# Kernel tuning notes

Measured on AMD Instinct MI355X. Metric: run time of the kernel, lower is better.

## Reference

```python
import jax, jax.numpy as jnp
import numpy as np

B, S, H, NH, DH, F, L = 4, 2048, 512, 8, 64, 2048, 4
ALPHA = 1.0   # config.lag_time_scale_alpha
EPS = 1e-12   # BERT layer_norm_eps
MS_PER_MIN = 60.0 * 1000.0


def setup_inputs() -> dict:
    key = jax.random.key(0)
    ks = jax.random.split(key, 24)
    p = lambda k, shape: (jax.random.normal(k, shape, jnp.float32) * 0.02)
    inp = {
        "query_states": jax.random.normal(ks[0], (B, S, H), jnp.float32),
        "attention_mask": jnp.zeros((B, 1, 1, S), jnp.float32),
        "position_bias": jax.random.normal(ks[1], (1, NH, S, S), jnp.float32) * 0.02,
        "timestamp": jnp.sort(jax.random.randint(ks[2], (B, S), 0, 36_000_000, jnp.int32), axis=-1),
        # stacked per-layer parameters (L leading dim)
        "wq": p(ks[3], (L, H, H)), "bq": jnp.zeros((L, H), jnp.float32),
        "wk": p(ks[4], (L, H, H)), "bk": jnp.zeros((L, H), jnp.float32),
        "wv": p(ks[5], (L, H, H)), "bv": jnp.zeros((L, H), jnp.float32),
        "wo": p(ks[6], (L, H, H)), "bo": jnp.zeros((L, H), jnp.float32),
        "ln1_g": jnp.ones((L, H), jnp.float32), "ln1_b": jnp.zeros((L, H), jnp.float32),
        "wi": p(ks[7], (L, H, F)), "bi": jnp.zeros((L, F), jnp.float32),
        "wo2": p(ks[8], (L, F, H)), "bo2": jnp.zeros((L, H), jnp.float32),
        "ln2_g": jnp.ones((L, H), jnp.float32), "ln2_b": jnp.zeros((L, H), jnp.float32),
    }
    return inp


def _ln(x, g, b):
    m = x.mean(-1, keepdims=True)
    v = ((x - m) ** 2).mean(-1, keepdims=True)
    return (x - m) / jnp.sqrt(v + EPS) * g + b


def reference(query_states, attention_mask, position_bias, timestamp,
              wq, bq, wk, bk, wv, bv, wo, bo, ln1_g, ln1_b,
              wi, bi, wo2, bo2, ln2_g, ln2_b):
    # encoder (is_decoder=False) lag-time scale: (B,1,S,S)
    lag = (timestamp[:, None, :, None] - timestamp[:, None, None, :]).astype(jnp.float32) / MS_PER_MIN
    scale = np.sqrt(DH).astype(np.float32) - ALPHA / (jnp.clip(lag, 0.0) + 1.0) + ALPHA

    x = query_states
    for l in range(L):
        def proj(w, b):
            return (x @ w + b).reshape(B, S, NH, DH).transpose(0, 2, 1, 3)  # (B,NH,S,DH)
        q, k, v = proj(wq[l], bq[l]), proj(wk[l], bk[l]), proj(wv[l], bv[l])
        scores = jnp.einsum('bhqd,bhkd->bhqk', q, k) / scale + position_bias + attention_mask
        probs = jax.nn.softmax(scores, axis=-1)
        ctx = jnp.einsum('bhqk,bhkd->bhqd', probs, v).transpose(0, 2, 1, 3).reshape(B, S, H)
        attn = _ln(ctx @ wo[l] + bo[l] + x, ln1_g[l], ln1_b[l])
        ffn = jax.nn.gelu(attn @ wi[l] + bi[l], approximate=False) @ wo2[l] + bo2[l]
        x = _ln(ffn + attn, ln2_g[l], ln2_b[l])
    return x
```

## Files before the change

kernel.cpp:

```cpp
#include <hip/hip_runtime.h>
#include <stdint.h>

typedef unsigned short u16;
using half8   = __attribute__((ext_vector_type(8))) _Float16;
using half4v  = __attribute__((ext_vector_type(4))) _Float16;
using half2v  = __attribute__((ext_vector_type(2))) _Float16;
using float4v = __attribute__((ext_vector_type(4))) float;

#define L2E 1.4426950408889634f

__device__ inline float4v f4zero() { float4v z = {0.f, 0.f, 0.f, 0.f}; return z; }

__device__ inline u16 f2h(float f) {
  union { _Float16 h; u16 u; } v; v.h = (_Float16)f; return v.u;
}
__device__ inline float h2f(u16 u) {
  union { u16 u; _Float16 h; } v; v.u = u; return (float)v.h;
}

__device__ inline half2v cvtpk(float a, float b) {
  return __builtin_bit_cast(half2v, __builtin_amdgcn_cvt_pkrtz(a, b));
}
__device__ inline _Float16 hexp2_(_Float16 x) {
  _Float16 r;
  asm("v_exp_f16 %0, %1" : "=v"(r) : "v"(x));
  return r;
}
__device__ inline float fdot2f(half2v a, float c) {
#if __has_builtin(__builtin_amdgcn_fdot2)
  typedef __attribute__((ext_vector_type(2))) __fp16 h2r;
  return __builtin_amdgcn_fdot2(__builtin_bit_cast(h2r, a),
                                __builtin_bit_cast(h2r, 0x3C003C00u), c, false);
#else
  return c + (float)a.x + (float)a.y;
#endif
}

__device__ inline void glds16(const u16* g, u16* lds_base, int lane) {
#if __has_builtin(__builtin_amdgcn_global_load_lds)
  (void)lane;
  __builtin_amdgcn_global_load_lds((const __attribute__((address_space(1))) void*)g,
                                   (__attribute__((address_space(3))) void*)lds_base,
                                   16, 0, 0);
#else
  *(uint4*)(lds_base + (size_t)lane * 8) = *(const uint4*)g;
#endif
}

__global__ __launch_bounds__(256) void transpose_cast_kernel(
    const float* __restrict__ in, u16* __restrict__ out, int K, int N, size_t out_ls) {
  __shared__ float tile[32][33];
  const int tx = threadIdx.x & 31, ty = threadIdx.x >> 5;
  in  += (size_t)blockIdx.z * K * N;
  out += (size_t)blockIdx.z * out_ls;
  const int n  = blockIdx.x * 32 + tx;
  const int k0 = blockIdx.y * 32;
#pragma unroll
  for (int j = 0; j < 32; j += 8)
    tile[ty + j][tx] = in[(size_t)(k0 + ty + j) * N + n];
  __syncthreads();
  const int k = k0 + tx;
  const int n0 = blockIdx.x * 32;
#pragma unroll
  for (int j = 0; j < 32; j += 8)
    out[(size_t)(n0 + ty + j) * K + k] = f2h(tile[tx][ty + j]);
}

__global__ __launch_bounds__(256) void cast_kernel(const float* __restrict__ in,
                                                   u16* __restrict__ out) {
  const int i = (blockIdx.x * 256 + threadIdx.x) * 4;
  float4 t = *(const float4*)(in + i);
  ushort4 o;
  o.x = f2h(t.x); o.y = f2h(t.y); o.z = f2h(t.z); o.w = f2h(t.w);
  *(ushort4*)(out + i) = o;
}

__global__ __launch_bounds__(256) void pb_tile_kernel(const float* __restrict__ pb,
                                                      u16* __restrict__ pbT) {
  const int g  = blockIdx.x * 256 + threadIdx.x;
  const int mm = g & 15;
  const int q  = (g >> 4) & 2047;
  const int kbh = g >> 15;
  const int kb = kbh & 31, h = kbh >> 5;
  const float* src = pb + ((size_t)h * 2048 + q) * 2048 + kb * 64 + mm;
  ushort4 o;
  o.x = f2h(src[0]  * L2E);
  o.y = f2h(src[16] * L2E);
  o.z = f2h(src[32] * L2E);
  o.w = f2h(src[48] * L2E);
  *(ushort4*)(pbT + ((size_t)(h * 32 + kb) * 2048 + q) * 64 + mm * 4) = o;
}

__global__ __launch_bounds__(256) void inv_tile_kernel(const int* __restrict__ ts,
                                                       u16* __restrict__ invT) {
  const int g  = blockIdx.x * 256 + threadIdx.x;
  const int mm = g & 15;
  const int q  = (g >> 4) & 2047;
  const int kb = (g >> 15) & 31;
  const int b  = g >> 20;
  const int tq = ts[b * 2048 + q];
  ushort4 o;
  u16* op = (u16*)&o;
#pragma unroll
  for (int nb = 0; nb < 4; nb++) {
    const int k = kb * 64 + nb * 16 + mm;
    const int du = tq - ts[b * 2048 + k];
    const float u = (du > 0) ? (float)du : 0.f;
    op[nb] = f2h(fmaf(u, L2E, 86561.70245333781f) *
                 __builtin_amdgcn_rcpf(fmaf(u, 9.f, 480000.f)));
  }
  *(ushort4*)(invT + ((size_t)(b * 32 + kb) * 2048 + q) * 64 + mm * 4) = o;
}

__global__ __launch_bounds__(256) void maskts_kernel(const float* __restrict__ mask,
                                                     const int* __restrict__ ts,
                                                     float* __restrict__ maskE,
                                                     float* __restrict__ tsf) {
  const int i = blockIdx.x * 256 + threadIdx.x;
  maskE[i] = mask[i] * L2E;
  tsf[i]   = (float)ts[i];
}

template <int BM, int BN, int NN, int KK, int EPI>
__global__ __launch_bounds__(256) void gemm_kernel(
    const u16* __restrict__ A, const u16* __restrict__ Wt,
    const float* __restrict__ b0, const float* __restrict__ b1, const float* __restrict__ b2,
    const u16* __restrict__ resid,
    void* __restrict__ o0, void* __restrict__ o1, void* __restrict__ o2) {
  constexpr int FI = BM / 32;
  constexpr int FJB = BN / 32;
  constexpr int FIW = BM / 32;
  constexpr int FJW = BN / 32;
  constexpr int NT = KK / 64;
  __shared__ __align__(16) u16 smem[2 * BM * 64 + 2 * BN * 64];
  u16* As0 = smem;
  u16* Bs0 = smem + 2 * BM * 64;
  const int tid = threadIdx.x, lane = tid & 63, wv = tid >> 6;
  const int quad = lane >> 4, mm = lane & 15;
  const int m0 = blockIdx.x * BM, n0 = blockIdx.y * BN;
  const int wm = (wv >> 1) * (BM / 2), wn = (wv & 1) * (BN / 2);
  const int srow = tid >> 3, slot = tid & 7;
  const int chunk = slot ^ (srow & 7);
  const u16* Ag = A  + (size_t)(m0 + srow) * KK + chunk * 8;
  const u16* Bg = Wt + (size_t)(n0 + srow) * KK + chunk * 8;
  const int sw = mm & 7;

  float4v acc[FIW][FJW];
#pragma unroll
  for (int i = 0; i < FIW; i++)
#pragma unroll
    for (int j = 0; j < FJW; j++) acc[i][j] = f4zero();

#pragma unroll
  for (int i = 0; i < FI; i++)
    glds16(Ag + (size_t)i * 32 * KK, As0 + (size_t)(wv * 8 + i * 32) * 64, lane);
#pragma unroll
  for (int j = 0; j < FJB; j++)
    glds16(Bg + (size_t)j * 32 * KK, Bs0 + (size_t)(wv * 8 + j * 32) * 64, lane);

  int cur = 0;
#pragma unroll 2
  for (int kt = 0; kt < NT; kt++) {
    __syncthreads();

    if (kt + 1 < NT) {
      const size_t ko = (size_t)(kt + 1) * 64;
#pragma unroll
      for (int i = 0; i < FI; i++)
        glds16(Ag + (size_t)i * 32 * KK + ko,
               As0 + (size_t)(cur ^ 1) * BM * 64 + (size_t)(wv * 8 + i * 32) * 64, lane);
#pragma unroll
      for (int j = 0; j < FJB; j++)
        glds16(Bg + (size_t)j * 32 * KK + ko,
               Bs0 + (size_t)(cur ^ 1) * BN * 64 + (size_t)(wv * 8 + j * 32) * 64, lane);
    }

    const u16* Ac = As0 + (size_t)cur * BM * 64;
    const u16* Bc = Bs0 + (size_t)cur * BN * 64;
#pragma unroll
    for (int ks = 0; ks < 2; ks++) {
      half8 a[FIW], b[FJW];
#pragma unroll
      for (int i = 0; i < FIW; i++)
        a[i] = *(const half8*)(Ac + (size_t)(wm + i * 16 + mm) * 64 + (size_t)((ks * 4 + quad) ^ sw) * 8);
#pragma unroll
      for (int j = 0; j < FJW; j++)
        b[j] = *(const half8*)(Bc + (size_t)(wn + j * 16 + mm) * 64 + (size_t)((ks * 4 + quad) ^ sw) * 8);
#pragma unroll
      for (int i = 0; i < FIW; i++)
#pragma unroll
        for (int j = 0; j < FJW; j++)
          acc[i][j] = __builtin_amdgcn_mfma_f32_16x16x32_f16(a[i], b[j], acc[i][j], 0, 0, 0);
    }
    cur ^= 1;
  }

  if constexpr (EPI == 4) {
    if (n0 >= 1024) {
      __syncthreads();
      u16* T = smem;
      const int h0 = (n0 >> 6) & 7;
      const int b_ = m0 >> 11, s_base = m0 & 2047;
#pragma unroll
      for (int j = 0; j < FJW; j++) {
        const int cn = wn + j * 16 + mm;
        const float bias = b2[(n0 & 511) + cn];
#pragma unroll
        for (int i = 0; i < FIW; i++)
#pragma unroll
          for (int r = 0; r < 4; r++) {
            const int gl = wm + i * 16 + quad * 4 + r;
            T[gl * 130 + cn] = f2h(acc[i][j][r] + bias);
          }
      }
      __syncthreads();
      const int rr = tid >> 1, shalf = tid & 1;
      const int hh = rr >> 6, dd = rr & 63;
      u16* outp = (u16*)o2 + ((size_t)((b_ * 8 + h0 + hh) * 64 + dd)) * 2048
                + s_base + shalf * 64;
#pragma unroll
      for (int g = 0; g < 8; g++) {
        union { u16 u[8]; uint4 v; } pk;
#pragma unroll
        for (int e = 0; e < 8; e++) {
          const int inner = g * 8 + e;
          const int sl = shalf * 64 + (((inner & 3) << 4) | (inner >> 2));
          pk.u[e] = T[sl * 130 + rr];
        }
        *(uint4*)(outp + g * 8) = pk.v;
      }
      return;
    }
  }

#pragma unroll
  for (int j = 0; j < FJW; j++) {
    const int gn = n0 + wn + j * 16 + mm;
    if (EPI == 4) {
      const int which = gn >> 9, col = gn & 511, h = (gn >> 6) & 7, d = gn & 63;
      const float* bp = (which == 0) ? b0 : b1;
      const float bias = bp[col];
      u16* dst = (which == 0) ? (u16*)o0 : (u16*)o1;
#pragma unroll
      for (int i = 0; i < FIW; i++)
#pragma unroll
        for (int r = 0; r < 4; r++) {
          const int gm = m0 + wm + i * 16 + quad * 4 + r;
          const int b_ = gm >> 11, s_ = gm & 2047;
          const float val = acc[i][j][r] + bias;
          dst[((size_t)((b_ * 8 + h) * 2048 + s_)) * 64 + d] = f2h(val);
        }
    } else {
      const float bias = b0[gn];
#pragma unroll
      for (int i = 0; i < FIW; i++)
#pragma unroll
        for (int r = 0; r < 4; r++) {
          const int gm = m0 + wm + i * 16 + quad * 4 + r;
          const float val = acc[i][j][r] + bias;
          const size_t idx = (size_t)gm * NN + gn;
          if (EPI == 2) {
            ((float*)o0)[idx] = val + h2f(resid[idx]);
          } else {
            const float z  = val * 0.70710678118654752f;
            const float az = fabsf(z);
            const float t  = __builtin_amdgcn_rcpf(1.0f + 0.3275911f * az);
            const float poly = t * (0.254829592f + t * (-0.284496736f +
                               t * (1.421413741f + t * (-1.453152027f + t * 1.061405429f))));
            const float e = __builtin_amdgcn_exp2f(-az * az * L2E);
            float erf_ = 1.0f - poly * e;
            erf_ = (z < 0.0f) ? -erf_ : erf_;
            ((u16*)o0)[idx] = f2h(val * 0.5f * (1.0f + erf_));
          }
        }
    }
  }
}

template <int TILED>
__global__ __launch_bounds__(512) void flash4_kernel(
    const u16* __restrict__ Q, const u16* __restrict__ Kb, const u16* __restrict__ Vt,
    const u16* __restrict__ pbT, const u16* __restrict__ invT,
    const float* __restrict__ pb32,
    const float* __restrict__ maskE, const float* __restrict__ tsf,
    u16* __restrict__ ctx) {
  __shared__ __align__(16) u16 Kls[2][64 * 64];
  __shared__ __align__(16) u16 Vls[2][64 * 64];
  __shared__ __align__(16) u16 P[8][16 * 64];
  const int tid = threadIdx.x, lane = tid & 63, w = tid >> 6;
  const int quad = lane >> 4, mm = lane & 15;
  const int bh = blockIdx.y, b_ = bh >> 3, h_ = bh & 7;
  const int q0 = blockIdx.x * 128 + w * 16;
  const size_t qk_base = (size_t)bh * 2048 * 64;
  const size_t v_base  = (size_t)bh * 64 * 2048;
  const int srow = lane >> 3, slot = lane & 7;
  const int chunk = slot ^ srow;
  const int sw = mm & 7;

  const u16* Kgl = Kb + qk_base + (size_t)(w * 8 + srow) * 64 + chunk * 8;
  const u16* Vgl = Vt + v_base + (size_t)(w * 8 + srow) * 2048 + chunk * 8;

  glds16(Kgl, &Kls[0][(w * 8) * 64], lane);
  glds16(Vgl, &Vls[0][(w * 8) * 64], lane);

  half8 aq[2];
#pragma unroll
  for (int t = 0; t < 2; t++)
    aq[t] = *(const half8*)(Q + qk_base + (size_t)(q0 + mm) * 64 + t * 32 + quad * 8);

  float tqf[4];
  if (TILED < 2) {
#pragma unroll
    for (int r = 0; r < 4; r++) tqf[r] = tsf[b_ * 2048 + q0 + quad * 4 + r];
  }

  float l_r[4] = {0.f, 0.f, 0.f, 0.f};
  float4v o[4];
#pragma unroll
  for (int ob = 0; ob < 4; ob++) o[ob] = f4zero();

  ushort4 pbc[4], invc[4]; float tkc[4], mkc[4];
  if (TILED >= 1) {
#pragma unroll
    for (int r = 0; r < 4; r++)
      pbc[r] = *(const ushort4*)(pbT + ((size_t)(h_ * 32) * 2048 + q0 + quad * 4 + r) * 64 + mm * 4);
  }
  if (TILED == 2) {
#pragma unroll
    for (int r = 0; r < 4; r++)
      invc[r] = *(const ushort4*)(invT + ((size_t)(b_ * 32) * 2048 + q0 + quad * 4 + r) * 64 + mm * 4);
  } else {
#pragma unroll
    for (int nb = 0; nb < 4; nb++) tkc[nb] = tsf[b_ * 2048 + nb * 16 + mm];
  }
#pragma unroll
  for (int nb = 0; nb < 4; nb++) mkc[nb] = maskE[b_ * 2048 + nb * 16 + mm];

  int cur = 0;
  for (int kt = 0; kt < 32; kt++) {
    const int k0 = kt * 64;
    __syncthreads();

    const int kn = (kt < 31) ? kt + 1 : kt;
    ushort4 pbn[4], invn[4]; float tkn[4], mkn[4];
    if (TILED >= 1) {
#pragma unroll
      for (int r = 0; r < 4; r++)
        pbn[r] = *(const ushort4*)(pbT + ((size_t)(h_ * 32 + kn) * 2048 + q0 + quad * 4 + r) * 64 + mm * 4);
    }
    if (TILED == 2) {
#pragma unroll
      for (int r = 0; r < 4; r++)
        invn[r] = *(const ushort4*)(invT + ((size_t)(b_ * 32 + kn) * 2048 + q0 + quad * 4 + r) * 64 + mm * 4);
    } else {
#pragma unroll
      for (int nb = 0; nb < 4; nb++) tkn[nb] = tsf[b_ * 2048 + kn * 64 + nb * 16 + mm];
    }
#pragma unroll
    for (int nb = 0; nb < 4; nb++) mkn[nb] = maskE[b_ * 2048 + kn * 64 + nb * 16 + mm];

    if (kt < 31) {
      const size_t ko = (size_t)(kt + 1) * 4096;
      const size_t vo = (size_t)(kt + 1) * 64;
      glds16(Kgl + ko, &Kls[cur ^ 1][(w * 8) * 64], lane);
      glds16(Vgl + vo, &Vls[cur ^ 1][(w * 8) * 64], lane);
    }

    const u16* Kc = Kls[cur];
    float4v s[4];
    __builtin_amdgcn_s_setprio(1);
#pragma unroll
    for (int nb = 0; nb < 4; nb++) {
      const half8 kf0 = *(const half8*)(Kc + (size_t)(nb * 16 + mm) * 64 + (size_t)(quad ^ sw) * 8);
      const half8 kf1 = *(const half8*)(Kc + (size_t)(nb * 16 + mm) * 64 + (size_t)((4 + quad) ^ sw) * 8);
      s[nb] = __builtin_amdgcn_mfma_f32_16x16x32_f16(aq[0], kf0, f4zero(), 0, 0, 0);
      s[nb] = __builtin_amdgcn_mfma_f32_16x16x32_f16(aq[1], kf1, s[nb], 0, 0, 0);
    }
    __builtin_amdgcn_s_setprio(0);

    const half2v mk01 = cvtpk(mkc[0], mkc[1]);
    const half2v mk23 = cvtpk(mkc[2], mkc[3]);
#pragma unroll
    for (int r = 0; r < 4; r++) {
      half2v pb01, pb23, iv01, iv23;
      if (TILED >= 1) {
        pb01 = *(const half2v*)&pbc[r].x;
        pb23 = *(const half2v*)&pbc[r].z;
      } else {
        float pv[4];
#pragma unroll
        for (int nb = 0; nb < 4; nb++)
          pv[nb] = pb32[((size_t)h_ * 2048 + q0 + quad * 4 + r) * 2048 + k0 + nb * 16 + mm] * L2E;
        pb01 = cvtpk(pv[0], pv[1]); pb23 = cvtpk(pv[2], pv[3]);
      }
      if (TILED == 2) {
        iv01 = *(const half2v*)&invc[r].x;
        iv23 = *(const half2v*)&invc[r].z;
      } else {
        float ivv[4];
#pragma unroll
        for (int nb = 0; nb < 4; nb++) {
          const float u = fmaxf(tqf[r] - tkc[nb], 0.f);
          ivv[nb] = fmaf(u, L2E, 86561.70245333781f) *
                    __builtin_amdgcn_rcpf(fmaf(u, 9.f, 480000.f));
        }
        iv01 = cvtpk(ivv[0], ivv[1]); iv23 = cvtpk(ivv[2], ivv[3]);
      }
      const half2v s01 = cvtpk(s[0][r], s[1][r]);
      const half2v s23 = cvtpk(s[2][r], s[3][r]);
      const half2v t01 = __builtin_elementwise_fma(s01, iv01, pb01 + mk01);
      const half2v t23 = __builtin_elementwise_fma(s23, iv23, pb23 + mk23);
      half2v p01, p23;
      p01.x = hexp2_(t01.x); p01.y = hexp2_(t01.y);
      p23.x = hexp2_(t23.x); p23.y = hexp2_(t23.y);
      l_r[r] = fdot2f(p01, l_r[r]);
      l_r[r] = fdot2f(p23, l_r[r]);
      const int prow = quad * 4 + r;
      union { half2v h2[2]; half4v h4; } uu;
      uu.h2[0] = p01; uu.h2[1] = p23;
      *(half4v*)((char*)P[w] + prow * 128 + ((mm * 8) ^ ((prow & 7) << 4))) = uu.h4;
    }

    const u16* Vc = Vls[cur];
    const char* Pb = (const char*)P[w] + mm * 128;
    const int pxor = (mm & 7) << 4;
    const half8 ap0 = *(const half8*)(Pb + ((quad * 16) ^ pxor));
    const half8 ap1 = *(const half8*)(Pb + ((64 + quad * 16) ^ pxor));
    __builtin_amdgcn_s_setprio(1);
#pragma unroll
    for (int ob = 0; ob < 4; ob++) {
      const half8 vf0 = *(const half8*)(Vc + (size_t)(ob * 16 + mm) * 64 + (size_t)(quad ^ sw) * 8);
      const half8 vf1 = *(const half8*)(Vc + (size_t)(ob * 16 + mm) * 64 + (size_t)((4 + quad) ^ sw) * 8);
      o[ob] = __builtin_amdgcn_mfma_f32_16x16x32_f16(ap0, vf0, o[ob], 0, 0, 0);
      o[ob] = __builtin_amdgcn_mfma_f32_16x16x32_f16(ap1, vf1, o[ob], 0, 0, 0);
    }
    __builtin_amdgcn_s_setprio(0);

#pragma unroll
    for (int r = 0; r < 4; r++) { pbc[r] = pbn[r]; invc[r] = invn[r]; }
#pragma unroll
    for (int nb = 0; nb < 4; nb++) { tkc[nb] = tkn[nb]; mkc[nb] = mkn[nb]; }
    cur ^= 1;
  }

#pragma unroll
  for (int r = 0; r < 4; r++) {
    float l = l_r[r];
#pragma unroll
    for (int sh = 1; sh < 16; sh <<= 1) l += __shfl_xor(l, sh, 64);
    const float rl = __builtin_amdgcn_rcpf(l);
    const int qrow = q0 + quad * 4 + r;
#pragma unroll
    for (int ob = 0; ob < 4; ob++)
      ctx[((size_t)b_ * 2048 + qrow) * 512 + h_ * 64 + ob * 16 + mm] = f2h(o[ob][r] * rl);
  }
}

__global__ __launch_bounds__(256) void ln_kernel(
    const float* __restrict__ in, const float* __restrict__ g, const float* __restrict__ bb,
    float* __restrict__ of, u16* __restrict__ obf) {
  const int lane = threadIdx.x & 63, w = threadIdx.x >> 6;
  const int row = blockIdx.x * 4 + w;
  const float* x = in + (size_t)row * 512;
  float v[8];
  const float4 t0 = *(const float4*)(x + lane * 8);
  const float4 t1 = *(const float4*)(x + lane * 8 + 4);
  v[0] = t0.x; v[1] = t0.y; v[2] = t0.z; v[3] = t0.w;
  v[4] = t1.x; v[5] = t1.y; v[6] = t1.z; v[7] = t1.w;
  float s = 0.f;
#pragma unroll
  for (int i = 0; i < 8; i++) s += v[i];
#pragma unroll
  for (int sh = 1; sh < 64; sh <<= 1) s += __shfl_xor(s, sh, 64);
  const float mean = s * (1.0f / 512.0f);
  float sq = 0.f;
#pragma unroll
  for (int i = 0; i < 8; i++) { const float d = v[i] - mean; sq += d * d; }
#pragma unroll
  for (int sh = 1; sh < 64; sh <<= 1) sq += __shfl_xor(sq, sh, 64);
  const float rstd = rsqrtf(sq * (1.0f / 512.0f) + 1e-12f);
#pragma unroll
  for (int i = 0; i < 8; i++) {
    const int col = lane * 8 + i;
    const float y = (v[i] - mean) * rstd * g[col] + bb[col];
    if (of) of[(size_t)row * 512 + col] = y;
    obf[(size_t)row * 512 + col] = f2h(y);
  }
}

extern "C" void kernel_launch(void* const* d_in, const int* in_sizes, int n_in,
                              void* d_out, int out_size, void* d_ws, size_t ws_size,
                              hipStream_t stream) {
  const float* x_in = (const float*)d_in[0];
  const float* mask = (const float*)d_in[1];
  const float* pb   = (const float*)d_in[2];
  const int*   ts   = (const int*)d_in[3];
  const float* wq = (const float*)d_in[4];  const float* bq = (const float*)d_in[5];
  const float* wk = (const float*)d_in[6];  const float* bk = (const float*)d_in[7];
  const float* wvp = (const float*)d_in[8]; const float* bv = (const float*)d_in[9];
  const float* wo = (const float*)d_in[10]; const float* bo = (const float*)d_in[11];
  const float* ln1g = (const float*)d_in[12]; const float* ln1b = (const float*)d_in[13];
  const float* wi = (const float*)d_in[14]; const float* bi = (const float*)d_in[15];
  const float* wo2 = (const float*)d_in[16]; const float* bo2 = (const float*)d_in[17];
  const float* ln2g = (const float*)d_in[18]; const float* ln2b = (const float*)d_in[19];

  char* ws = (char*)d_ws;
  const size_t o_wqkv  = 0;
  const size_t o_woT   = 6291456;
  const size_t o_wiT   = 8388608;
  const size_t o_wo2T  = 16777216;
  const size_t o_maskE = 25165824;
  const size_t o_tsf   = 25198592;
  const size_t o_xbf   = 25231360;
  const size_t o_qb    = 33619968;
  const size_t o_kb    = 42008576;
  const size_t o_vb    = 50397184;
  const size_t o_ctx   = 58785792;
  const size_t o_attnb = 67174400;
  const size_t o_tmp   = 75563008;
  const size_t o_pbT   = 92340224;
  const size_t o_invT  = 159449088;
  const int tiled = (ws_size >= o_invT + 33554432ull) ? 2
                  : (ws_size >= o_pbT + 67108864ull) ? 1 : 0;

  u16*   wqkvT = (u16*)(ws + o_wqkv);
  u16*   woT   = (u16*)(ws + o_woT);
  u16*   wiT   = (u16*)(ws + o_wiT);
  u16*   wo2T  = (u16*)(ws + o_wo2T);
  float* maskE = (float*)(ws + o_maskE);
  float* tsf   = (float*)(ws + o_tsf);
  u16*   xbf   = (u16*)(ws + o_xbf);
  u16*   qb    = (u16*)(ws + o_qb);
  u16*   kb    = (u16*)(ws + o_kb);
  u16*   vb    = (u16*)(ws + o_vb);
  u16*   ctx   = (u16*)(ws + o_ctx);
  u16*   hb    = (u16*)(ws + o_qb);
  u16*   attnb = (u16*)(ws + o_attnb);
  float* tmp   = (float*)(ws + o_tmp);
  u16*   pbT   = (u16*)(ws + o_pbT);
  u16*   invT  = (u16*)(ws + o_invT);

  const dim3 blk(256);
  const dim3 blk512(512);
  transpose_cast_kernel<<<dim3(16, 16, 4), blk, 0, stream>>>(wq,  wqkvT,          512, 512, 786432);
  transpose_cast_kernel<<<dim3(16, 16, 4), blk, 0, stream>>>(wk,  wqkvT + 262144, 512, 512, 786432);
  transpose_cast_kernel<<<dim3(16, 16, 4), blk, 0, stream>>>(wvp, wqkvT + 524288, 512, 512, 786432);
  transpose_cast_kernel<<<dim3(16, 16, 4), blk, 0, stream>>>(wo,  woT,  512, 512,  262144);
  transpose_cast_kernel<<<dim3(64, 16, 4), blk, 0, stream>>>(wi,  wiT,  512, 2048, 1048576);
  transpose_cast_kernel<<<dim3(16, 64, 4), blk, 0, stream>>>(wo2, wo2T, 2048, 512, 1048576);
  maskts_kernel<<<32, blk, 0, stream>>>(mask, ts, maskE, tsf);
  cast_kernel<<<4096, blk, 0, stream>>>(x_in, xbf);
  if (tiled >= 1) pb_tile_kernel<<<32768, blk, 0, stream>>>(pb, pbT);
  if (tiled == 2) inv_tile_kernel<<<16384, blk, 0, stream>>>(ts, invT);

  for (int l = 0; l < 4; l++) {
    gemm_kernel<128, 128, 1536, 512, 4><<<dim3(64, 12), blk, 0, stream>>>(
        xbf, wqkvT + (size_t)l * 786432, bq + l * 512, bk + l * 512, bv + l * 512,
        nullptr, qb, kb, vb);
    if (tiled == 2)
      flash4_kernel<2><<<dim3(16, 32), blk512, 0, stream>>>(qb, kb, vb, pbT, invT, pb, maskE, tsf, ctx);
    else if (tiled == 1)
      flash4_kernel<1><<<dim3(16, 32), blk512, 0, stream>>>(qb, kb, vb, pbT, nullptr, pb, maskE, tsf, ctx);
    else
      flash4_kernel<0><<<dim3(16, 32), blk512, 0, stream>>>(qb, kb, vb, nullptr, nullptr, pb, maskE, tsf, ctx);
    gemm_kernel<128, 64, 512, 512, 2><<<dim3(64, 8), blk, 0, stream>>>(
        ctx, woT + (size_t)l * 262144, bo + l * 512, nullptr, nullptr, xbf,
        tmp, nullptr, nullptr);
    ln_kernel<<<2048, blk, 0, stream>>>(tmp, ln1g + l * 512, ln1b + l * 512, nullptr, attnb);
    gemm_kernel<128, 128, 2048, 512, 3><<<dim3(64, 16), blk, 0, stream>>>(
        attnb, wiT + (size_t)l * 1048576, bi + l * 2048, nullptr, nullptr, nullptr,
        hb, nullptr, nullptr);
    gemm_kernel<128, 64, 512, 2048, 2><<<dim3(64, 8), blk, 0, stream>>>(
        hb, wo2T + (size_t)l * 1048576, bo2 + l * 512, nullptr, nullptr, attnb,
        tmp, nullptr, nullptr);
    ln_kernel<<<2048, blk, 0, stream>>>(tmp, ln2g + l * 512, ln2b + l * 512,
                                        (l == 3) ? (float*)d_out : nullptr, xbf);
  }
  (void)in_sizes; (void)n_in; (void)out_size;
}
```

Measured before the change: 1.159 ms.

## Add 256x128-tile 512-thread GEMM for QKV and FFN-up projections

Adds a new gemm8_kernel that uses 8 waves and a 256x128 output tile (each wave computing 64x64) for the QKV projection and the FFN up-projection. The old kernel's V-transpose epilogue is split into two half passes through shared memory. The goal is more operand reuse per LDS load and fewer blocks. The trade-offs are higher register pressure, half as many blocks (384/512), and a single-buffered K loop with two barriers per step instead of the previous double buffering, which may expose load latency.

Result: faster. 1.123 ms (-3.1%).

```diff
diff --git a/kernel.cpp b/kernel.cpp
--- a/kernel.cpp
+++ b/kernel.cpp
@@ -195,85 +195,166 @@
     cur ^= 1;
   }
 
+#pragma unroll
+  for (int j = 0; j < FJW; j++) {
+    const int gn = n0 + wn + j * 16 + mm;
+    const float bias = b0[gn];
+#pragma unroll
+    for (int i = 0; i < FIW; i++)
+#pragma unroll
+      for (int r = 0; r < 4; r++) {
+        const int gm = m0 + wm + i * 16 + quad * 4 + r;
+        const float val = acc[i][j][r] + bias;
+        const size_t idx = (size_t)gm * NN + gn;
+        if (EPI == 2) {
+          ((float*)o0)[idx] = val + h2f(resid[idx]);
+        } else {
+          const float z  = val * 0.70710678118654752f;
+          const float az = fabsf(z);
+          const float t  = __builtin_amdgcn_rcpf(1.0f + 0.3275911f * az);
+          const float poly = t * (0.254829592f + t * (-0.284496736f +
+                             t * (1.421413741f + t * (-1.453152027f + t * 1.061405429f))));
+          const float e = __builtin_amdgcn_exp2f(-az * az * L2E);
+          float erf_ = 1.0f - poly * e;
+          erf_ = (z < 0.0f) ? -erf_ : erf_;
+          ((u16*)o0)[idx] = f2h(val * 0.5f * (1.0f + erf_));
+        }
+      }
+  }
+  (void)b1; (void)b2; (void)o1; (void)o2;
+}
+
+template <int NN, int KK, int EPI>
+__global__ __launch_bounds__(512) void gemm8_kernel(
+    const u16* __restrict__ A, const u16* __restrict__ Wt,
+    const float* __restrict__ b0, const float* __restrict__ b1, const float* __restrict__ b2,
+    void* __restrict__ o0, void* __restrict__ o1, void* __restrict__ o2) {
+  __shared__ __align__(16) u16 smem[256 * 64 + 128 * 64];
+  u16* As = smem;
+  u16* Bs = smem + 256 * 64;
+  const int tid = threadIdx.x, lane = tid & 63, wv = tid >> 6;
+  const int quad = lane >> 4, mm = lane & 15;
+  const int m0 = blockIdx.x * 256, n0 = blockIdx.y * 128;
+  const int wm = (wv >> 1) * 64, wn = (wv & 1) * 64;
+  const int srow = tid >> 3, slot = tid & 7;
+  const int chunk = slot ^ (srow & 7);
+  const u16* Ag = A  + (size_t)(m0 + srow) * KK + chunk * 8;
+  const u16* Bg = Wt + (size_t)(n0 + srow) * KK + chunk * 8;
+  const int sw = mm & 7;
+
+  float4v acc[4][4];
+#pragma unroll
+  for (int i = 0; i < 4; i++)
+#pragma unroll
+    for (int j = 0; j < 4; j++) acc[i][j] = f4zero();
+
+  for (int kte = 0; kte < KK; kte += 64) {
+#pragma unroll
+    for (int p = 0; p < 4; p++)
+      glds16(Ag + (size_t)(p * 64) * KK + kte, As + (size_t)(p * 64 + wv * 8) * 64, lane);
+#pragma unroll
+    for (int p = 0; p < 2; p++)
+      glds16(Bg + (size_t)(p * 64) * KK + kte, Bs + (size_t)(p * 64 + wv * 8) * 64, lane);
+    __syncthreads();
+
+#pragma unroll
+    for (int ks = 0; ks < 2; ks++) {
+      half8 a[4], b[4];
+#pragma unroll
+      for (int i = 0; i < 4; i++)
+        a[i] = *(const half8*)(As + (size_t)(wm + i * 16 + mm) * 64 + (size_t)((ks * 4 + quad) ^ sw) * 8);
+#pragma unroll
+      for (int j = 0; j < 4; j++)
+        b[j] = *(const half8*)(Bs + (size_t)(wn + j * 16 + mm) * 64 + (size_t)((ks * 4 + quad) ^ sw) * 8);
+#pragma unroll
+      for (int i = 0; i < 4; i++)
+#pragma unroll
+        for (int j = 0; j < 4; j++)
+          acc[i][j] = __builtin_amdgcn_mfma_f32_16x16x32_f16(a[i], b[j], acc[i][j], 0, 0, 0);
+    }
+    __syncthreads();
+  }
+
   if constexpr (EPI == 4) {
     if (n0 >= 1024) {
-      __syncthreads();
+      const int b_ = m0 >> 11, s_base = m0 & 2047;
+      const int h0 = (n0 >> 6) & 7;
       u16* T = smem;
-      const int h0 = (n0 >> 6) & 7;
-      const int b_ = m0 >> 11, s_base = m0 & 2047;
-#pragma unroll
-      for (int j = 0; j < FJW; j++) {
-        const int cn = wn + j * 16 + mm;
-        const float bias = b2[(n0 & 511) + cn];
-#pragma unroll
-        for (int i = 0; i < FIW; i++)
-#pragma unroll
-          for (int r = 0; r < 4; r++) {
-            const int gl = wm + i * 16 + quad * 4 + r;
-            T[gl * 130 + cn] = f2h(acc[i][j][r] + bias);
+#pragma unroll
+      for (int hp = 0; hp < 2; hp++) {
+        __syncthreads();
+        if ((wv >> 2) == hp) {
+          const int lm = wm & 127;
+#pragma unroll
+          for (int j = 0; j < 4; j++) {
+            const int cn = wn + j * 16 + mm;
+            const float bias = b2[(n0 & 511) + cn];
+#pragma unroll
+            for (int i = 0; i < 4; i++)
+#pragma unroll
+              for (int r = 0; r < 4; r++)
+                T[(lm + i * 16 + quad * 4 + r) * 130 + cn] = f2h(acc[i][j][r] + bias);
           }
-      }
-      __syncthreads();
-      const int rr = tid >> 1, shalf = tid & 1;
-      const int hh = rr >> 6, dd = rr & 63;
-      u16* outp = (u16*)o2 + ((size_t)((b_ * 8 + h0 + hh) * 64 + dd)) * 2048
-                + s_base + shalf * 64;
-#pragma unroll
-      for (int g = 0; g < 8; g++) {
-        union { u16 u[8]; uint4 v; } pk;
-#pragma unroll
-        for (int e = 0; e < 8; e++) {
-          const int inner = g * 8 + e;
-          const int sl = shalf * 64 + (((inner & 3) << 4) | (inner >> 2));
-          pk.u[e] = T[sl * 130 + rr];
         }
-        *(uint4*)(outp + g * 8) = pk.v;
+        __syncthreads();
+        const int rr = tid >> 2, sq = tid & 3;
+        const int hh = rr >> 6, dd = rr & 63;
+        u16* outp = (u16*)o2 + ((size_t)((b_ * 8 + h0 + hh) * 64 + dd)) * 2048
+                  + s_base + hp * 128 + sq * 32;
+#pragma unroll
+        for (int g = 0; g < 4; g++) {
+          union { u16 u[8]; uint4 v; } pk;
+#pragma unroll
+          for (int e = 0; e < 8; e++) {
+            const int sl = sq * 32 + g * 8 + e;
+            const int tl = (sl & 64) + (((sl & 3) << 4) | ((sl & 63) >> 2));
+            pk.u[e] = T[tl * 130 + rr];
+          }
+          *(uint4*)(outp + g * 8) = pk.v;
+        }
       }
       return;
     }
-  }
-
-#pragma unroll
-  for (int j = 0; j < FJW; j++) {
-    const int gn = n0 + wn + j * 16 + mm;
-    if (EPI == 4) {
+#pragma unroll
+    for (int j = 0; j < 4; j++) {
+      const int gn = n0 + wn + j * 16 + mm;
       const int which = gn >> 9, col = gn & 511, h = (gn >> 6) & 7, d = gn & 63;
       const float* bp = (which == 0) ? b0 : b1;
       const float bias = bp[col];
       u16* dst = (which == 0) ? (u16*)o0 : (u16*)o1;
 #pragma unroll
-      for (int i = 0; i < FIW; i++)
+      for (int i = 0; i < 4; i++)
 #pragma unroll
         for (int r = 0; r < 4; r++) {
           const int gm = m0 + wm + i * 16 + quad * 4 + r;
           const int b_ = gm >> 11, s_ = gm & 2047;
-          const float val = acc[i][j][r] + bias;
-          dst[((size_t)((b_ * 8 + h) * 2048 + s_)) * 64 + d] = f2h(val);
+          dst[((size_t)((b_ * 8 + h) * 2048 + s_)) * 64 + d] = f2h(acc[i][j][r] + bias);
         }
-    } else {
-      const float bias = b0[gn];
-#pragma unroll
-      for (int i = 0; i < FIW; i++)
-#pragma unroll
-        for (int r = 0; r < 4; r++) {
-          const int gm = m0 + wm + i * 16 + quad * 4 + r;
-          const float val = acc[i][j][r] + bias;
-          const size_t idx = (size_t)gm * NN + gn;
-          if (EPI == 2) {
-            ((float*)o0)[idx] = val + h2f(resid[idx]);
-          } else {
-            const float z  = val * 0.70710678118654752f;
-            const float az = fabsf(z);
-            const float t  = __builtin_amdgcn_rcpf(1.0f + 0.3275911f * az);
-            const float poly = t * (0.254829592f + t * (-0.284496736f +
-                               t * (1.421413741f + t * (-1.453152027f + t * 1.061405429f))));
-            const float e = __builtin_amdgcn_exp2f(-az * az * L2E);
-            float erf_ = 1.0f - poly * e;
-            erf_ = (z < 0.0f) ? -erf_ : erf_;
-            ((u16*)o0)[idx] = f2h(val * 0.5f * (1.0f + erf_));
-          }
-        }
-    }
+    }
+    return;
+  }
+
+#pragma unroll
+  for (int j = 0; j < 4; j++) {
+    const int gn = n0 + wn + j * 16 + mm;
+    const float bias = b0[gn];
+#pragma unroll
+    for (int i = 0; i < 4; i++)
+#pragma unroll
+      for (int r = 0; r < 4; r++) {
+        const int gm = m0 + wm + i * 16 + quad * 4 + r;
+        const float val = acc[i][j][r] + bias;
+        const size_t idx = (size_t)gm * NN + gn;
+        const float z  = val * 0.70710678118654752f;
+        const float az = fabsf(z);
+        const float t  = __builtin_amdgcn_rcpf(1.0f + 0.3275911f * az);
+        const float poly = t * (0.254829592f + t * (-0.284496736f +
+                           t * (1.421413741f + t * (-1.453152027f + t * 1.061405429f))));
+        const float e = __builtin_amdgcn_exp2f(-az * az * L2E);
+        float erf_ = 1.0f - poly * e;
+        erf_ = (z < 0.0f) ? -erf_ : erf_;
+        ((u16*)o0)[idx] = f2h(val * 0.5f * (1.0f + erf_));
+      }
   }
 }
 
@@ -554,9 +635,9 @@
   if (tiled == 2) inv_tile_kernel<<<16384, blk, 0, stream>>>(ts, invT);
 
   for (int l = 0; l < 4; l++) {
-    gemm_kernel<128, 128, 1536, 512, 4><<<dim3(64, 12), blk, 0, stream>>>(
+    gemm8_kernel<1536, 512, 4><<<dim3(32, 12), blk512, 0, stream>>>(
         xbf, wqkvT + (size_t)l * 786432, bq + l * 512, bk + l * 512, bv + l * 512,
-        nullptr, qb, kb, vb);
+        qb, kb, vb);
     if (tiled == 2)
       flash4_kernel<2><<<dim3(16, 32), blk512, 0, stream>>>(qb, kb, vb, pbT, invT, pb, maskE, tsf, ctx);
     else if (tiled == 1)
@@ -567,8 +648,8 @@
         ctx, woT + (size_t)l * 262144, bo + l * 512, nullptr, nullptr, xbf,
         tmp, nullptr, nullptr);
     ln_kernel<<<2048, blk, 0, stream>>>(tmp, ln1g + l * 512, ln1b + l * 512, nullptr, attnb);
-    gemm_kernel<128, 128, 2048, 512, 3><<<dim3(64, 16), blk, 0, stream>>>(
-        attnb, wiT + (size_t)l * 1048576, bi + l * 2048, nullptr, nullptr, nullptr,
+    gemm8_kernel<2048, 512, 3><<<dim3(32, 16), blk512, 0, stream>>>(
+        attnb, wiT + (size_t)l * 1048576, bi + l * 2048, nullptr, nullptr,
         hb, nullptr, nullptr);
     gemm_kernel<128, 64, 512, 2048, 2><<<dim3(64, 8), blk, 0, stream>>>(
         hb, wo2T + (size_t)l * 1048576, bo2 + l * 512, nullptr, nullptr, attnb,
```
